# Optimization experiments

Hardware: AMD Instinct MI355X
Metric: run time of the kernel (lower is better)

Reference implementation:

```python
import jax, jax.numpy as jnp
import numpy as np

B, L, C, NH = 512, 129, 512, 8
TAU = 1.0


def layer_norm(x, g, b, eps=1e-5):
    m = x.mean(-1, keepdims=True)
    v = x.var(-1, keepdims=True)
    return (x - m) / jnp.sqrt(v + eps) * g + b


def attn_pool(tokens, query, in_w, in_b, out_w, out_b, ln_g, ln_b):
    # single-query multi-head attention pooling (nn.MultiheadAttention, batch_first)
    Bn, Ln, Cn = tokens.shape
    dh = Cn // NH
    Wq, Wk, Wv = jnp.split(in_w, 3, axis=0)
    bq, bk, bv = jnp.split(in_b, 3)
    q = (query[0, 0] @ Wq.T + bq).reshape(NH, dh)           # (H, dh), shared across batch
    k = (tokens @ Wk.T + bk).reshape(Bn, Ln, NH, dh)
    v = (tokens @ Wv.T + bv).reshape(Bn, Ln, NH, dh)
    scale = 1.0 / jnp.sqrt(jnp.asarray(dh, tokens.dtype))
    scores = jnp.einsum('hd,blhd->bhl', q, k) * scale       # (B, H, L)
    w = jax.nn.softmax(scores, axis=-1)
    out = jnp.einsum('bhl,blhd->bhd', w, v).reshape(Bn, Cn)
    out = out @ out_w.T + out_b
    return layer_norm(out, ln_g, ln_b)


def entropy(feat):
    fa = jnp.abs(feat) + 1e-8
    p = fa / fa.sum(-1, keepdims=True)
    return -(p * jnp.log(p + 1e-8)).sum(-1)


def setup_inputs() -> dict:
    key = jax.random.key(0)
    ks = jax.random.split(key, 20)
    s = C ** -0.5
    inp = {
        'rgb_tokens': jax.random.normal(ks[0], (B, L, C), jnp.float32),
        'nir_tokens': jax.random.normal(ks[1], (B, L, C), jnp.float32),
        'tir_tokens': jax.random.normal(ks[2], (B, L, C), jnp.float32),
        'rgb_query': s * jax.random.normal(ks[3], (1, 1, C), jnp.float32),
        'nir_query': s * jax.random.normal(ks[4], (1, 1, C), jnp.float32),
        'tir_query': s * jax.random.normal(ks[5], (1, 1, C), jnp.float32),
        'in_proj_w': 0.02 * jax.random.normal(ks[6], (3 * C, C), jnp.float32),
        'in_proj_b': jnp.zeros((3 * C,), jnp.float32),
        'out_proj_w': 0.02 * jax.random.normal(ks[7], (C, C), jnp.float32),
        'out_proj_b': jnp.zeros((C,), jnp.float32),
        'attn_ln_g': jnp.ones((C,), jnp.float32),
        'attn_ln_b': jnp.zeros((C,), jnp.float32),
        'ent_w': 0.02 * jax.random.normal(ks[8], (C, C), jnp.float32),
        'ent_b': jnp.zeros((C,), jnp.float32),
        'gate_w1': 0.02 * jax.random.normal(ks[9], (C, 3 * C), jnp.float32),
        'gate_b1': jnp.zeros((C,), jnp.float32),
        'gate_ln_g': jnp.ones((C,), jnp.float32),
        'gate_ln_b': jnp.zeros((C,), jnp.float32),
        'gate_w2': 0.02 * jax.random.normal(ks[10], (3, C), jnp.float32),
        'gate_b2': jnp.zeros((3,), jnp.float32),
        'alpha_raw': jnp.asarray(0.5, jnp.float32),
        'enh_w': 0.02 * jax.random.normal(ks[11], (C, C), jnp.float32),
        'enh_b': jnp.zeros((C,), jnp.float32),
        'enh_ln_g': jnp.ones((C,), jnp.float32),
        'enh_ln_b': jnp.zeros((C,), jnp.float32),
    }
    return inp


def reference(rgb_tokens, nir_tokens, tir_tokens, rgb_query, nir_query, tir_query,
              in_proj_w, in_proj_b, out_proj_w, out_proj_b, attn_ln_g, attn_ln_b,
              ent_w, ent_b, gate_w1, gate_b1, gate_ln_g, gate_ln_b, gate_w2, gate_b2,
              alpha_raw, enh_w, enh_b, enh_ln_g, enh_ln_b):
    ap = lambda t, q: attn_pool(t, q, in_proj_w, in_proj_b, out_proj_w, out_proj_b, attn_ln_g, attn_ln_b)
    h_rgb, h_nir, h_tir = ap(rgb_tokens, rgb_query), ap(nir_tokens, nir_query), ap(tir_tokens, tir_query)
    H_r, H_n, H_t = entropy(h_rgb), entropy(h_nir), entropy(h_tir)
    z = lambda h: (h @ ent_w.T + ent_b).mean(-1)
    scores = jnp.stack([z(h_rgb) * jnp.exp(-H_r / TAU),
                        z(h_nir) * jnp.exp(-H_n / TAU),
                        z(h_tir) * jnp.exp(-H_t / TAU)], axis=-1)   # (B, 3)
    ew = jax.nn.softmax(scores, axis=-1)
    h_entropy = ew[:, 0:1] * h_rgb + ew[:, 1:2] * h_nir + ew[:, 2:3] * h_tir
    h_concat = jnp.concatenate([h_rgb, h_nir, h_tir], axis=-1)      # (B, 3C)
    g = jax.nn.relu(layer_norm(h_concat @ gate_w1.T + gate_b1, gate_ln_g, gate_ln_b))
    gates = jax.nn.sigmoid(g @ gate_w2.T + gate_b2)                  # (B, 3)
    h_importance = gates[:, 0:1] * h_rgb + gates[:, 1:2] * h_nir + gates[:, 2:3] * h_tir
    alpha = jax.nn.sigmoid(alpha_raw)
    h_fused = alpha * h_entropy + (1.0 - alpha) * h_importance
    h_enh = layer_norm(h_fused @ enh_w.T + enh_b, enh_ln_g, enh_ln_b)
    return jnp.concatenate([h_rgb + h_enh, h_nir + h_enh, h_tir + h_enh], axis=-1)  # (B, 3C)
```

## Files before the change

### kernel.cpp

```cpp
#include <hip/hip_runtime.h>
#include <cstdint>

#define WS_U      0
#define WS_C0     12288
#define WS_ENTBM  12312
#define WS_ENTP   12320
#define WS_P      16416
#define WS_OUT2   WS_P
#define WS_GPRE   (WS_P + 786432)
#define WS_HFUSED (WS_P + 1572864)
#define WS_ENHPRE (WS_P + 1835008)
#define WS_VOUT   (WS_P + 6291456)
#define WS_HCAT   (WS_VOUT + 786432)
#define WS_H      (WS_HCAT + 786432)
#define WS_Z      (WS_H + 1536)

__device__ __forceinline__ float blk_sum4(float v, float* red, int lane, int wave) {
#pragma unroll
  for (int off = 32; off; off >>= 1) v += __shfl_xor(v, off);
  __syncthreads();
  if (lane == 0) red[wave] = v;
  __syncthreads();
  return red[0] + red[1] + red[2] + red[3];
}

__global__ __launch_bounds__(256) void prep_kernel(
    const float* __restrict__ qrgb, const float* __restrict__ qnir, const float* __restrict__ qtir,
    const float* __restrict__ inw, const float* __restrict__ inb,
    const float* __restrict__ entw, const float* __restrict__ entb,
    float* __restrict__ ws)
{
  const int m = blockIdx.x, h = blockIdx.y;
  const int tid = threadIdx.x, lane = tid & 63, wave = tid >> 6;
  __shared__ float qvl[64];
  __shared__ float red[4];

  if (m == 3) {
    const float* base = entw + (size_t)h * 64 * 512;
    float acc0 = 0.f, acc1 = 0.f;
#pragma unroll 8
    for (int r = 0; r < 64; r++) {
      acc0 += base[(size_t)r * 512 + tid];
      acc1 += base[(size_t)r * 512 + tid + 256];
    }
    ws[WS_ENTP + h * 512 + tid] = acc0;
    ws[WS_ENTP + h * 512 + tid + 256] = acc1;
    return;
  }

  const float* qry = (m == 0) ? qrgb : (m == 1) ? qnir : qtir;
  float4 q0 = *(const float4*)(qry + 4 * lane);
  float4 q1 = *(const float4*)(qry + 256 + 4 * lane);
#pragma unroll 4
  for (int dd = 0; dd < 16; dd++) {
    const int d = wave * 16 + dd;
    const float* wr = inw + (size_t)(h * 64 + d) * 512;
    float4 w0 = *(const float4*)(wr + 4 * lane);
    float4 w1 = *(const float4*)(wr + 256 + 4 * lane);
    float p = w0.x * q0.x + w0.y * q0.y + w0.z * q0.z + w0.w * q0.w
            + w1.x * q1.x + w1.y * q1.y + w1.z * q1.z + w1.w * q1.w;
#pragma unroll
    for (int off = 32; off; off >>= 1) p += __shfl_xor(p, off);
    if (lane == 0) qvl[d] = p + inb[h * 64 + d];
  }
  __syncthreads();
  float acc0 = 0.f, acc1 = 0.f;
  const float* wk = inw + (size_t)(512 + h * 64) * 512;
#pragma unroll 8
  for (int d = 0; d < 64; d++) {
    float qq = qvl[d];
    acc0 = fmaf(qq, wk[(size_t)d * 512 + tid], acc0);
    acc1 = fmaf(qq, wk[(size_t)d * 512 + tid + 256], acc1);
  }
  ws[WS_U + m * 4096 + h * 512 + tid] = 0.125f * acc0;
  ws[WS_U + m * 4096 + h * 512 + tid + 256] = 0.125f * acc1;
  if (m == 0 && h == 0) {
    float v = entb[tid] + entb[tid + 256];
    float s = blk_sum4(v, red, lane, wave);
    if (tid == 0) ws[WS_ENTBM] = s * (1.f / 512.f);
  }
}

__global__ __launch_bounds__(256) void attn_pool_kernel(
    const float* __restrict__ trgb, const float* __restrict__ tnir, const float* __restrict__ ttir,
    const float* __restrict__ ws, float* __restrict__ Pout)
{
  const int b = blockIdx.x, m = blockIdx.y;
  const int tid = threadIdx.x, lane = tid & 63, wave = tid >> 6;
  const float* tok = ((m == 0) ? trgb : (m == 1) ? tnir : ttir) + (size_t)b * 129 * 512;
  const float* u = ws + WS_U + m * 4096;

  __shared__ float sc[8][132];
  __shared__ float lacc[4][2][512];

  const int b0 = lane & 1, b1 = (lane >> 1) & 1, b2 = (lane >> 2) & 1;
  const int b3 = (lane >> 3) & 1, b4 = (lane >> 4) & 1;
  const int r_own = (b0 << 1) | b1;
  const int h_own = (b2 << 2) | (b3 << 1) | b4;

  const int wbase = wave * 32;

#define LOADB(L0, A0, C0, A1, C1, A2, C2, A3, C3)                         \
  do {                                                                    \
    int r0_ = (L0), r1_ = (L0) + 1, r2_ = (L0) + 2, r3_ = (L0) + 3;       \
    if (r1_ > 128) r1_ = 128;                                             \
    if (r2_ > 128) r2_ = 128;                                             \
    if (r3_ > 128) r3_ = 128;                                             \
    const float* p0_ = tok + (size_t)r0_ * 512 + 4 * lane;                \
    const float* p1_ = tok + (size_t)r1_ * 512 + 4 * lane;                \
    const float* p2_ = tok + (size_t)r2_ * 512 + 4 * lane;                \
    const float* p3_ = tok + (size_t)r3_ * 512 + 4 * lane;                \
    A0 = *(const float4*)p0_; C0 = *(const float4*)(p0_ + 256);           \
    A1 = *(const float4*)p1_; C1 = *(const float4*)(p1_ + 256);           \
    A2 = *(const float4*)p2_; C2 = *(const float4*)(p2_ + 256);           \
    A3 = *(const float4*)p3_; C3 = *(const float4*)(p3_ + 256);           \
  } while (0)

  auto score_batch = [&](int l0, bool tail,
                         float4 A0, float4 C0, float4 A1, float4 C1,
                         float4 A2, float4 C2, float4 A3, float4 C3) {
    float x[32];
#pragma unroll
    for (int h = 0; h < 8; h++) {
      float4 U0 = *(const float4*)(u + h * 512 + 4 * lane);
      float4 U1 = *(const float4*)(u + h * 512 + 256 + 4 * lane);
      x[h]      = A0.x * U0.x + A0.y * U0.y + A0.z * U0.z + A0.w * U0.w
                + C0.x * U1.x + C0.y * U1.y + C0.z * U1.z + C0.w * U1.w;
      x[8 + h]  = A1.x * U0.x + A1.y * U0.y + A1.z * U0.z + A1.w * U0.w
                + C1.x * U1.x + C1.y * U1.y + C1.z * U1.z + C1.w * U1.w;
      x[16 + h] = A2.x * U0.x + A2.y * U0.y + A2.z * U0.z + A2.w * U0.w
                + C2.x * U1.x + C2.y * U1.y + C2.z * U1.z + C2.w * U1.w;
      x[24 + h] = A3.x * U0.x + A3.y * U0.y + A3.z * U0.z + A3.w * U0.w
                + C3.x * U1.x + C3.y * U1.y + C3.z * U1.z + C3.w * U1.w;
    }
#define MERGE_STAGE(n, M, bit)                                  \
    _Pragma("unroll")                                           \
    for (int j = 0; j < (n) / 2; j++) {                         \
      float keep = (bit) ? x[j + (n) / 2] : x[j];               \
      float send = (bit) ? x[j] : x[j + (n) / 2];               \
      x[j] = keep + __shfl_xor(send, (M));                      \
    }
    MERGE_STAGE(32, 1, b0)
    MERGE_STAGE(16, 2, b1)
    MERGE_STAGE(8, 4, b2)
    MERGE_STAGE(4, 8, b3)
    MERGE_STAGE(2, 16, b4)
#undef MERGE_STAGE
    float T = x[0] + __shfl_xor(x[0], 32);
    if (lane < 32 && (!tail || r_own == 0))
      sc[h_own][l0 + r_own] = T;
  };

  {
    float4 A0, C0, A1, C1, A2, C2, A3, C3;
    float4 N0, D0, N1, D1, N2, D2, N3, D3;
    LOADB(wbase, A0, C0, A1, C1, A2, C2, A3, C3);
    for (int bt = 0; bt < 8; bt++) {
      if (bt < 7) LOADB(wbase + 4 * bt + 4, N0, D0, N1, D1, N2, D2, N3, D3);
      score_batch(wbase + 4 * bt, false, A0, C0, A1, C1, A2, C2, A3, C3);
      A0 = N0; C0 = D0; A1 = N1; C1 = D1;
      A2 = N2; C2 = D2; A3 = N3; C3 = D3;
    }
    if (wave == 0) {
      LOADB(128, A0, C0, A1, C1, A2, C2, A3, C3);
      score_batch(128, true, A0, C0, A1, C1, A2, C2, A3, C3);
    }
  }
  __syncthreads();

#pragma unroll
  for (int hh = 0; hh < 2; hh++) {
    const int h = wave * 2 + hh;
    float x0 = sc[h][lane];
    float x1 = sc[h][64 + lane];
    float x2 = (lane == 0) ? sc[h][128] : -3.0e38f;
    float mx = fmaxf(fmaxf(x0, x1), x2);
#pragma unroll
    for (int off = 32; off; off >>= 1) mx = fmaxf(mx, __shfl_xor(mx, off));
    float e0 = __expf(x0 - mx), e1 = __expf(x1 - mx);
    float e2 = (lane == 0) ? __expf(x2 - mx) : 0.f;
    float s = e0 + e1 + e2;
#pragma unroll
    for (int off = 32; off; off >>= 1) s += __shfl_xor(s, off);
    float inv = 1.f / s;
    sc[h][lane] = e0 * inv;
    sc[h][64 + lane] = e1 * inv;
    if (lane == 0) sc[h][128] = e2 * inv;
  }
  __syncthreads();

  float acc[8][8];
#pragma unroll
  for (int h = 0; h < 8; h++)
#pragma unroll
    for (int j = 0; j < 8; j++) acc[h][j] = 0.f;
  {
    float4 pa0, pc0, pa1, pc1, qa0, qc0, qa1, qc1;
    {
      const float* p0 = tok + (size_t)wbase * 512 + 4 * lane;
      const float* p1 = tok + (size_t)(wbase + 1) * 512 + 4 * lane;
      pa0 = *(const float4*)p0; pc0 = *(const float4*)(p0 + 256);
      pa1 = *(const float4*)p1; pc1 = *(const float4*)(p1 + 256);
    }
    for (int g = 0; g < 16; g++) {
      if (g < 15) {
        const float* p0 = tok + (size_t)(wbase + 2 * g + 2) * 512 + 4 * lane;
        const float* p1 = tok + (size_t)(wbase + 2 * g + 3) * 512 + 4 * lane;
        qa0 = *(const float4*)p0; qc0 = *(const float4*)(p0 + 256);
        qa1 = *(const float4*)p1; qc1 = *(const float4*)(p1 + 256);
      }
#pragma unroll
      for (int h = 0; h < 8; h++) {
        float2 w2 = *(const float2*)&sc[h][wbase + 2 * g];
        acc[h][0] = fmaf(w2.x, pa0.x, acc[h][0]);
        acc[h][1] = fmaf(w2.x, pa0.y, acc[h][1]);
        acc[h][2] = fmaf(w2.x, pa0.z, acc[h][2]);
        acc[h][3] = fmaf(w2.x, pa0.w, acc[h][3]);
        acc[h][4] = fmaf(w2.x, pc0.x, acc[h][4]);
        acc[h][5] = fmaf(w2.x, pc0.y, acc[h][5]);
        acc[h][6] = fmaf(w2.x, pc0.z, acc[h][6]);
        acc[h][7] = fmaf(w2.x, pc0.w, acc[h][7]);
        acc[h][0] = fmaf(w2.y, pa1.x, acc[h][0]);
        acc[h][1] = fmaf(w2.y, pa1.y, acc[h][1]);
        acc[h][2] = fmaf(w2.y, pa1.z, acc[h][2]);
        acc[h][3] = fmaf(w2.y, pa1.w, acc[h][3]);
        acc[h][4] = fmaf(w2.y, pc1.x, acc[h][4]);
        acc[h][5] = fmaf(w2.y, pc1.y, acc[h][5]);
        acc[h][6] = fmaf(w2.y, pc1.z, acc[h][6]);
        acc[h][7] = fmaf(w2.y, pc1.w, acc[h][7]);
      }
      pa0 = qa0; pc0 = qc0; pa1 = qa1; pc1 = qc1;
    }
    if (wave == 0) {
      const float* p0 = tok + (size_t)128 * 512 + 4 * lane;
      float4 ta = *(const float4*)p0;
      float4 tc = *(const float4*)(p0 + 256);
#pragma unroll
      for (int h = 0; h < 8; h++) {
        float wt = sc[h][128];
        acc[h][0] = fmaf(wt, ta.x, acc[h][0]);
        acc[h][1] = fmaf(wt, ta.y, acc[h][1]);
        acc[h][2] = fmaf(wt, ta.z, acc[h][2]);
        acc[h][3] = fmaf(wt, ta.w, acc[h][3]);
        acc[h][4] = fmaf(wt, tc.x, acc[h][4]);
        acc[h][5] = fmaf(wt, tc.y, acc[h][5]);
        acc[h][6] = fmaf(wt, tc.z, acc[h][6]);
        acc[h][7] = fmaf(wt, tc.w, acc[h][7]);
      }
    }
  }
#undef LOADB

  float* po = Pout + (size_t)(m * 512 + b) * 4096 + 2 * tid;
#pragma unroll
  for (int hb = 0; hb < 8; hb += 2) {
    __syncthreads();
#pragma unroll
    for (int hh = 0; hh < 2; hh++) {
      const int h = hb + hh;
      *(float4*)&lacc[wave][hh][4 * lane] =
          make_float4(acc[h][0], acc[h][1], acc[h][2], acc[h][3]);
      *(float4*)&lacc[wave][hh][256 + 4 * lane] =
          make_float4(acc[h][4], acc[h][5], acc[h][6], acc[h][7]);
    }
    __syncthreads();
#pragma unroll
    for (int hh = 0; hh < 2; hh++) {
      const int h = hb + hh;
      float2 x0 = *(const float2*)&lacc[0][hh][2 * tid];
      float2 x1 = *(const float2*)&lacc[1][hh][2 * tid];
      float2 x2 = *(const float2*)&lacc[2][hh][2 * tid];
      float2 x3 = *(const float2*)&lacc[3][hh][2 * tid];
      *(float2*)(po + h * 512) =
          make_float2(x0.x + x1.x + x2.x + x3.x, x0.y + x1.y + x2.y + x3.y);
    }
  }
}

__global__ __launch_bounds__(256) void gemm_bt_kernel(
    const float* __restrict__ A, const float* __restrict__ B,
    const float* __restrict__ bias, float* __restrict__ C,
    int K, int lda, int ldb, int ldc,
    long sA, long sB, long sC, int sBias, int addBias)
{
  A += (long)blockIdx.z * sA;
  B += (long)blockIdx.z * sB;
  C += (long)blockIdx.z * sC;
  const float* bp = bias + (long)blockIdx.z * sBias;
  __shared__ float As[32][68];
  __shared__ float Bs[32][68];
  const int tid = threadIdx.x;
  const int tx = tid & 15, ty = tid >> 4;
  const int rowL = tid >> 3;
  const int colv = (tid & 7) << 2;
  const int m0 = blockIdx.x * 64, n0 = blockIdx.y * 64;
  float acc[4][4] = {};
  for (int k0 = 0; k0 < K; k0 += 32) {
#pragma unroll
    for (int it = 0; it < 2; it++) {
      const int r = rowL + it * 32;
      float4 v = *(const float4*)(A + (size_t)(m0 + r) * lda + k0 + colv);
      As[colv + 0][r] = v.x; As[colv + 1][r] = v.y; As[colv + 2][r] = v.z; As[colv + 3][r] = v.w;
      float4 w = *(const float4*)(B + (size_t)(n0 + r) * ldb + k0 + colv);
      Bs[colv + 0][r] = w.x; Bs[colv + 1][r] = w.y; Bs[colv + 2][r] = w.z; Bs[colv + 3][r] = w.w;
    }
    __syncthreads();
#pragma unroll
    for (int k = 0; k < 32; k++) {
      float4 a4 = *(const float4*)&As[k][ty * 4];
      float4 b4 = *(const float4*)&Bs[k][tx * 4];
      acc[0][0] += a4.x * b4.x; acc[0][1] += a4.x * b4.y; acc[0][2] += a4.x * b4.z; acc[0][3] += a4.x * b4.w;
      acc[1][0] += a4.y * b4.x; acc[1][1] += a4.y * b4.y; acc[1][2] += a4.y * b4.z; acc[1][3] += a4.y * b4.w;
      acc[2][0] += a4.z * b4.x; acc[2][1] += a4.z * b4.y; acc[2][2] += a4.z * b4.z; acc[2][3] += a4.z * b4.w;
      acc[3][0] += a4.w * b4.x; acc[3][1] += a4.w * b4.y; acc[3][2] += a4.w * b4.z; acc[3][3] += a4.w * b4.w;
    }
    __syncthreads();
  }
  float4 bv = make_float4(0.f, 0.f, 0.f, 0.f);
  if (addBias) bv = *(const float4*)(bp + n0 + tx * 4);
#pragma unroll
  for (int i = 0; i < 4; i++) {
    float4 o;
    o.x = acc[i][0] + bv.x; o.y = acc[i][1] + bv.y;
    o.z = acc[i][2] + bv.z; o.w = acc[i][3] + bv.w;
    *(float4*)(C + (size_t)(m0 + ty * 4 + i) * ldc + n0 + tx * 4) = o;
  }
}

__global__ __launch_bounds__(256) void ln_ent_kernel(
    const float* __restrict__ out2,
    const float* __restrict__ lng, const float* __restrict__ lnb,
    const float* __restrict__ ws, float* __restrict__ hcat,
    float* __restrict__ Hout, float* __restrict__ zout)
{
  const int r = blockIdx.x;
  const int mod = r >> 9, b = r & 511;
  const int tid = threadIdx.x, lane = tid & 63, wave = tid >> 6;
  __shared__ float red[4];
  const float* x = out2 + (size_t)r * 512;
  float2 v = *(const float2*)(x + 2 * tid);
  float s = blk_sum4(v.x + v.y, red, lane, wave);
  float sq = blk_sum4(v.x * v.x + v.y * v.y, red, lane, wave);
  float mean = s * (1.f / 512.f);
  float var = sq * (1.f / 512.f) - mean * mean;
  float rstd = rsqrtf(var + 1e-5f);
  float2 g = *(const float2*)(lng + 2 * tid);
  float2 bb = *(const float2*)(lnb + 2 * tid);
  float h0 = (v.x - mean) * rstd * g.x + bb.x;
  float h1 = (v.y - mean) * rstd * g.y + bb.y;
  *(float2*)(hcat + (size_t)b * 1536 + mod * 512 + 2 * tid) = make_float2(h0, h1);
  float2 ep = make_float2(0.f, 0.f);
#pragma unroll
  for (int j = 0; j < 8; j++) {
    float2 t = *(const float2*)(ws + WS_ENTP + j * 512 + 2 * tid);
    ep.x += t.x; ep.y += t.y;
  }
  ep.x *= (1.f / 512.f); ep.y *= (1.f / 512.f);
  float fa0 = fabsf(h0) + 1e-8f, fa1 = fabsf(h1) + 1e-8f;
  float S = blk_sum4(fa0 + fa1, red, lane, wave);
  float zz = blk_sum4(h0 * ep.x + h1 * ep.y, red, lane, wave);
  float invS = 1.f / S;
  float p0 = fa0 * invS, p1 = fa1 * invS;
  float t = blk_sum4(p0 * logf(p0 + 1e-8f) + p1 * logf(p1 + 1e-8f), red, lane, wave);
  if (tid == 0) {
    Hout[mod * 512 + b] = -t;
    zout[mod * 512 + b] = zz + ws[WS_ENTBM];
  }
}

__global__ __launch_bounds__(256) void gate_fuse_kernel(
    const float* __restrict__ gpre, const float* __restrict__ glng, const float* __restrict__ glnb,
    const float* __restrict__ gw2, const float* __restrict__ gb2, const float* __restrict__ gb1,
    const float* __restrict__ araw, const float* __restrict__ hcat,
    const float* __restrict__ H, const float* __restrict__ z,
    float* __restrict__ hfused)
{
  const int b = blockIdx.x;
  const int tid = threadIdx.x, lane = tid & 63, wave = tid >> 6;
  __shared__ float red[4];
  float2 v;
  {
    float2 p0 = *(const float2*)(gpre + (size_t)b * 512 + 2 * tid);
    float2 p1 = *(const float2*)(gpre + 262144 + (size_t)b * 512 + 2 * tid);
    float2 p2 = *(const float2*)(gpre + 524288 + (size_t)b * 512 + 2 * tid);
    float2 bi = *(const float2*)(gb1 + 2 * tid);
    v.x = p0.x + p1.x + p2.x + bi.x;
    v.y = p0.y + p1.y + p2.y + bi.y;
  }
  float s = blk_sum4(v.x + v.y, red, lane, wave);
  float sq = blk_sum4(v.x * v.x + v.y * v.y, red, lane, wave);
  float mean = s * (1.f / 512.f), var = sq * (1.f / 512.f) - mean * mean;
  float rstd = rsqrtf(var + 1e-5f);
  float2 g = *(const float2*)(glng + 2 * tid);
  float2 bb = *(const float2*)(glnb + 2 * tid);
  float g0 = fmaxf((v.x - mean) * rstd * g.x + bb.x, 0.f);
  float g1 = fmaxf((v.y - mean) * rstd * g.y + bb.y, 0.f);
  float d0 = blk_sum4(g0 * gw2[2 * tid] + g1 * gw2[2 * tid + 1], red, lane, wave);
  float d1 = blk_sum4(g0 * gw2[512 + 2 * tid] + g1 * gw2[512 + 2 * tid + 1], red, lane, wave);
  float d2 = blk_sum4(g0 * gw2[1024 + 2 * tid] + g1 * gw2[1024 + 2 * tid + 1], red, lane, wave);
  float ga0 = 1.f / (1.f + __expf(-(d0 + gb2[0])));
  float ga1 = 1.f / (1.f + __expf(-(d1 + gb2[1])));
  float ga2 = 1.f / (1.f + __expf(-(d2 + gb2[2])));
  float sc0 = z[b] * __expf(-H[b]);
  float sc1 = z[512 + b] * __expf(-H[512 + b]);
  float sc2 = z[1024 + b] * __expf(-H[1024 + b]);
  float mxs = fmaxf(sc0, fmaxf(sc1, sc2));
  float e0 = __expf(sc0 - mxs), e1 = __expf(sc1 - mxs), e2 = __expf(sc2 - mxs);
  float inv = 1.f / (e0 + e1 + e2);
  e0 *= inv; e1 *= inv; e2 *= inv;
  float alpha = 1.f / (1.f + __expf(-araw[0]));
  const float* hb = hcat + (size_t)b * 1536 + 2 * tid;
  float2 hr = *(const float2*)hb;
  float2 hn = *(const float2*)(hb + 512);
  float2 ht = *(const float2*)(hb + 1024);
  float2 o;
  o.x = alpha * (e0 * hr.x + e1 * hn.x + e2 * ht.x)
      + (1.f - alpha) * (ga0 * hr.x + ga1 * hn.x + ga2 * ht.x);
  o.y = alpha * (e0 * hr.y + e1 * hn.y + e2 * ht.y)
      + (1.f - alpha) * (ga0 * hr.y + ga1 * hn.y + ga2 * ht.y);
  *(float2*)(hfused + (size_t)b * 512 + 2 * tid) = o;
}

__global__ __launch_bounds__(256) void final_out_kernel(
    const float* __restrict__ epre, const float* __restrict__ enb,
    const float* __restrict__ elng, const float* __restrict__ elnb,
    const float* __restrict__ hcat, float* __restrict__ out)
{
  const int b = blockIdx.x;
  const int tid = threadIdx.x, lane = tid & 63, wave = tid >> 6;
  __shared__ float red[4];
  float2 v;
  {
    float2 p0 = *(const float2*)(epre + (size_t)b * 512 + 2 * tid);
    float2 p1 = *(const float2*)(epre + 262144 + (size_t)b * 512 + 2 * tid);
    float2 bi = *(const float2*)(enb + 2 * tid);
    v.x = p0.x + p1.x + bi.x;
    v.y = p0.y + p1.y + bi.y;
  }
  float s = blk_sum4(v.x + v.y, red, lane, wave);
  float sq = blk_sum4(v.x * v.x + v.y * v.y, red, lane, wave);
  float mean = s * (1.f / 512.f), var = sq * (1.f / 512.f) - mean * mean;
  float rstd = rsqrtf(var + 1e-5f);
  float2 g = *(const float2*)(elng + 2 * tid);
  float2 bb = *(const float2*)(elnb + 2 * tid);
  float e0 = (v.x - mean) * rstd * g.x + bb.x;
  float e1 = (v.y - mean) * rstd * g.y + bb.y;
  const float* hb = hcat + (size_t)b * 1536 + 2 * tid;
  float* ob = out + (size_t)b * 1536 + 2 * tid;
#pragma unroll
  for (int mm = 0; mm < 3; mm++) {
    float2 hv = *(const float2*)(hb + mm * 512);
    *(float2*)(ob + mm * 512) = make_float2(hv.x + e0, hv.y + e1);
  }
}

extern "C" void kernel_launch(void* const* d_in, const int* in_sizes, int n_in,
                              void* d_out, int out_size, void* d_ws, size_t ws_size,
                              hipStream_t stream)
{
  const float* trgb = (const float*)d_in[0];
  const float* tnir = (const float*)d_in[1];
  const float* ttir = (const float*)d_in[2];
  const float* qrgb = (const float*)d_in[3];
  const float* qnir = (const float*)d_in[4];
  const float* qtir = (const float*)d_in[5];
  const float* inw  = (const float*)d_in[6];
  const float* inb  = (const float*)d_in[7];
  const float* outw = (const float*)d_in[8];
  const float* outb = (const float*)d_in[9];
  const float* alng = (const float*)d_in[10];
  const float* alnb = (const float*)d_in[11];
  const float* entw = (const float*)d_in[12];
  const float* entb = (const float*)d_in[13];
  const float* gw1  = (const float*)d_in[14];
  const float* gb1  = (const float*)d_in[15];
  const float* glng = (const float*)d_in[16];
  const float* glnb = (const float*)d_in[17];
  const float* gw2  = (const float*)d_in[18];
  const float* gb2  = (const float*)d_in[19];
  const float* araw = (const float*)d_in[20];
  const float* enw  = (const float*)d_in[21];
  const float* enb  = (const float*)d_in[22];
  const float* elng = (const float*)d_in[23];
  const float* elnb = (const float*)d_in[24];
  float* ws = (float*)d_ws;
  float* out = (float*)d_out;

  hipLaunchKernelGGL(prep_kernel, dim3(4, 8), dim3(256), 0, stream,
                     qrgb, qnir, qtir, inw, inb, entw, entb, ws);
  hipLaunchKernelGGL(attn_pool_kernel, dim3(512, 3), dim3(256), 0, stream,
                     trgb, tnir, ttir, ws, ws + WS_P);
  hipLaunchKernelGGL(gemm_bt_kernel, dim3(24, 1, 8), dim3(256), 0, stream,
                     ws + WS_P, inw + (size_t)1024 * 512, inb + 1024, ws + WS_VOUT,
                     512, 4096, 512, 512,
                     (long)512, (long)64 * 512, (long)64, 64, 1);
  hipLaunchKernelGGL(gemm_bt_kernel, dim3(24, 8, 1), dim3(256), 0, stream,
                     ws + WS_VOUT, outw, outb, ws + WS_OUT2,
                     512, 512, 512, 512, 0L, 0L, 0L, 0, 1);
  hipLaunchKernelGGL(ln_ent_kernel, dim3(1536), dim3(256), 0, stream,
                     ws + WS_OUT2, alng, alnb, ws, ws + WS_HCAT, ws + WS_H, ws + WS_Z);
  hipLaunchKernelGGL(gemm_bt_kernel, dim3(8, 8, 3), dim3(256), 0, stream,
                     ws + WS_HCAT, gw1, gb1, ws + WS_GPRE,
                     512, 1536, 1536, 512,
                     (long)512, (long)512, (long)262144, 0, 0);
  hipLaunchKernelGGL(gate_fuse_kernel, dim3(512), dim3(256), 0, stream,
                     ws + WS_GPRE, glng, glnb, gw2, gb2, gb1, araw,
                     ws + WS_HCAT, ws + WS_H, ws + WS_Z, ws + WS_HFUSED);
  hipLaunchKernelGGL(gemm_bt_kernel, dim3(8, 8, 2), dim3(256), 0, stream,
                     ws + WS_HFUSED, enw, enb, ws + WS_ENHPRE,
                     256, 512, 512, 512,
                     (long)256, (long)256, (long)262144, 0, 0);
  hipLaunchKernelGGL(final_out_kernel, dim3(512), dim3(256), 0, stream,
                     ws + WS_ENHPRE, enb, elng, elnb, ws + WS_HCAT, out);
}
```

Baseline: 287.5 us.

## Split attention pooling into separate score and weighted-sum kernels

The fused attention-pool kernel is split in two. The first kernel computes the scores and softmax and writes the per-head weights to the workspace. The second kernel reloads those weights and has each wave accumulate two heads over all 129 token rows. This removes the cross-wave shared-memory reduction and cuts register pressure, aiming for higher occupancy. The cost is a second full pass over the token tensors from a separate launch, plus four-fold redundant token reads per block, since every wave now streams the whole token tile.

```diff
diff --git a/kernel.cpp b/kernel.cpp
--- a/kernel.cpp
+++ b/kernel.cpp
@@ -81,7 +81,7 @@
   }
 }
 
-__global__ __launch_bounds__(256) void attn_pool_kernel(
+__global__ __launch_bounds__(256) void attn_score_kernel(
     const float* __restrict__ trgb, const float* __restrict__ tnir, const float* __restrict__ ttir,
     const float* __restrict__ ws, float* __restrict__ Pout)
 {
@@ -91,13 +91,11 @@
   const float* u = ws + WS_U + m * 4096;
 
   __shared__ float sc[8][132];
-  __shared__ float lacc[4][2][512];
 
   const int b0 = lane & 1, b1 = (lane >> 1) & 1, b2 = (lane >> 2) & 1;
   const int b3 = (lane >> 3) & 1, b4 = (lane >> 4) & 1;
   const int r_own = (b0 << 1) | b1;
   const int h_own = (b2 << 2) | (b3 << 1) | b4;
-
   const int wbase = wave * 32;
 
 #define LOADB(L0, A0, C0, A1, C1, A2, C2, A3, C3)                         \
@@ -166,8 +164,10 @@
       score_batch(128, true, A0, C0, A1, C1, A2, C2, A3, C3);
     }
   }
+#undef LOADB
   __syncthreads();
 
+  float* wout = Pout + (size_t)(m * 512 + b) * 4096;
 #pragma unroll
   for (int hh = 0; hh < 2; hh++) {
     const int h = wave * 2 + hh;
@@ -183,98 +183,80 @@
 #pragma unroll
     for (int off = 32; off; off >>= 1) s += __shfl_xor(s, off);
     float inv = 1.f / s;
-    sc[h][lane] = e0 * inv;
-    sc[h][64 + lane] = e1 * inv;
-    if (lane == 0) sc[h][128] = e2 * inv;
-  }
+    wout[h * 132 + lane] = e0 * inv;
+    wout[h * 132 + 64 + lane] = e1 * inv;
+    if (lane == 0) wout[h * 132 + 128] = e2 * inv;
+  }
+}
+
+__global__ __launch_bounds__(256) void attn_pool_kernel(
+    const float* __restrict__ trgb, const float* __restrict__ tnir, const float* __restrict__ ttir,
+    float* __restrict__ Pout)
+{
+  const int b = blockIdx.x, m = blockIdx.y;
+  const int tid = threadIdx.x, lane = tid & 63, wave = tid >> 6;
+  const float* tok = ((m == 0) ? trgb : (m == 1) ? tnir : ttir) + (size_t)b * 129 * 512;
+  float* prow = Pout + (size_t)(m * 512 + b) * 4096;
+
+  __shared__ float sc[8][132];
+  for (int i = tid; i < 1056; i += 256) ((float*)sc)[i] = prow[i];
   __syncthreads();
 
-  float acc[8][8];
-#pragma unroll
-  for (int h = 0; h < 8; h++)
-#pragma unroll
-    for (int j = 0; j < 8; j++) acc[h][j] = 0.f;
-  {
-    float4 pa0, pc0, pa1, pc1, qa0, qc0, qa1, qc1;
-    {
-      const float* p0 = tok + (size_t)wbase * 512 + 4 * lane;
-      const float* p1 = tok + (size_t)(wbase + 1) * 512 + 4 * lane;
-      pa0 = *(const float4*)p0; pc0 = *(const float4*)(p0 + 256);
-      pa1 = *(const float4*)p1; pc1 = *(const float4*)(p1 + 256);
-    }
-    for (int g = 0; g < 16; g++) {
-      if (g < 15) {
-        const float* p0 = tok + (size_t)(wbase + 2 * g + 2) * 512 + 4 * lane;
-        const float* p1 = tok + (size_t)(wbase + 2 * g + 3) * 512 + 4 * lane;
-        qa0 = *(const float4*)p0; qc0 = *(const float4*)(p0 + 256);
-        qa1 = *(const float4*)p1; qc1 = *(const float4*)(p1 + 256);
-      }
-#pragma unroll
-      for (int h = 0; h < 8; h++) {
-        float2 w2 = *(const float2*)&sc[h][wbase + 2 * g];
-        acc[h][0] = fmaf(w2.x, pa0.x, acc[h][0]);
-        acc[h][1] = fmaf(w2.x, pa0.y, acc[h][1]);
-        acc[h][2] = fmaf(w2.x, pa0.z, acc[h][2]);
-        acc[h][3] = fmaf(w2.x, pa0.w, acc[h][3]);
-        acc[h][4] = fmaf(w2.x, pc0.x, acc[h][4]);
-        acc[h][5] = fmaf(w2.x, pc0.y, acc[h][5]);
-        acc[h][6] = fmaf(w2.x, pc0.z, acc[h][6]);
-        acc[h][7] = fmaf(w2.x, pc0.w, acc[h][7]);
-        acc[h][0] = fmaf(w2.y, pa1.x, acc[h][0]);
-        acc[h][1] = fmaf(w2.y, pa1.y, acc[h][1]);
-        acc[h][2] = fmaf(w2.y, pa1.z, acc[h][2]);
-        acc[h][3] = fmaf(w2.y, pa1.w, acc[h][3]);
-        acc[h][4] = fmaf(w2.y, pc1.x, acc[h][4]);
-        acc[h][5] = fmaf(w2.y, pc1.y, acc[h][5]);
-        acc[h][6] = fmaf(w2.y, pc1.z, acc[h][6]);
-        acc[h][7] = fmaf(w2.y, pc1.w, acc[h][7]);
-      }
-      pa0 = qa0; pc0 = qc0; pa1 = qa1; pc1 = qc1;
-    }
-    if (wave == 0) {
-      const float* p0 = tok + (size_t)128 * 512 + 4 * lane;
-      float4 ta = *(const float4*)p0;
-      float4 tc = *(const float4*)(p0 + 256);
-#pragma unroll
-      for (int h = 0; h < 8; h++) {
-        float wt = sc[h][128];
-        acc[h][0] = fmaf(wt, ta.x, acc[h][0]);
-        acc[h][1] = fmaf(wt, ta.y, acc[h][1]);
-        acc[h][2] = fmaf(wt, ta.z, acc[h][2]);
-        acc[h][3] = fmaf(wt, ta.w, acc[h][3]);
-        acc[h][4] = fmaf(wt, tc.x, acc[h][4]);
-        acc[h][5] = fmaf(wt, tc.y, acc[h][5]);
-        acc[h][6] = fmaf(wt, tc.z, acc[h][6]);
-        acc[h][7] = fmaf(wt, tc.w, acc[h][7]);
-      }
-    }
-  }
-#undef LOADB
-
-  float* po = Pout + (size_t)(m * 512 + b) * 4096 + 2 * tid;
-#pragma unroll
-  for (int hb = 0; hb < 8; hb += 2) {
-    __syncthreads();
-#pragma unroll
-    for (int hh = 0; hh < 2; hh++) {
-      const int h = hb + hh;
-      *(float4*)&lacc[wave][hh][4 * lane] =
-          make_float4(acc[h][0], acc[h][1], acc[h][2], acc[h][3]);
-      *(float4*)&lacc[wave][hh][256 + 4 * lane] =
-          make_float4(acc[h][4], acc[h][5], acc[h][6], acc[h][7]);
-    }
-    __syncthreads();
-#pragma unroll
-    for (int hh = 0; hh < 2; hh++) {
-      const int h = hb + hh;
-      float2 x0 = *(const float2*)&lacc[0][hh][2 * tid];
-      float2 x1 = *(const float2*)&lacc[1][hh][2 * tid];
-      float2 x2 = *(const float2*)&lacc[2][hh][2 * tid];
-      float2 x3 = *(const float2*)&lacc[3][hh][2 * tid];
-      *(float2*)(po + h * 512) =
-          make_float2(x0.x + x1.x + x2.x + x3.x, x0.y + x1.y + x2.y + x3.y);
-    }
-  }
+  const int h0 = wave * 2, h1 = h0 + 1;
+  float4 acc00 = make_float4(0.f, 0.f, 0.f, 0.f);
+  float4 acc01 = make_float4(0.f, 0.f, 0.f, 0.f);
+  float4 acc10 = make_float4(0.f, 0.f, 0.f, 0.f);
+  float4 acc11 = make_float4(0.f, 0.f, 0.f, 0.f);
+
+#define LDROW(rr, Av, Cv)                                         \
+  do {                                                            \
+    const float* p_ = tok + (size_t)(rr) * 512 + 4 * lane;        \
+    Av = *(const float4*)p_; Cv = *(const float4*)(p_ + 256);     \
+  } while (0)
+
+#define POOLR(Av, Cv, l)                                          \
+  do {                                                            \
+    float w0_ = sc[h0][l], w1_ = sc[h1][l];                       \
+    acc00.x = fmaf(w0_, Av.x, acc00.x);                           \
+    acc00.y = fmaf(w0_, Av.y, acc00.y);                           \
+    acc00.z = fmaf(w0_, Av.z, acc00.z);                           \
+    acc00.w = fmaf(w0_, Av.w, acc00.w);                           \
+    acc01.x = fmaf(w0_, Cv.x, acc01.x);                           \
+    acc01.y = fmaf(w0_, Cv.y, acc01.y);                           \
+    acc01.z = fmaf(w0_, Cv.z, acc01.z);                           \
+    acc01.w = fmaf(w0_, Cv.w, acc01.w);                           \
+    acc10.x = fmaf(w1_, Av.x, acc10.x);                           \
+    acc10.y = fmaf(w1_, Av.y, acc10.y);                           \
+    acc10.z = fmaf(w1_, Av.z, acc10.z);                           \
+    acc10.w = fmaf(w1_, Av.w, acc10.w);                           \
+    acc11.x = fmaf(w1_, Cv.x, acc11.x);                           \
+    acc11.y = fmaf(w1_, Cv.y, acc11.y);                           \
+    acc11.z = fmaf(w1_, Cv.z, acc11.z);                           \
+    acc11.w = fmaf(w1_, Cv.w, acc11.w);                           \
+  } while (0)
+
+  float4 A0, C0, A1, C1, A2, C2, A3, C3;
+  LDROW(0, A0, C0); LDROW(1, A1, C1); LDROW(2, A2, C2); LDROW(3, A3, C3);
+  for (int g = 0; g < 32; g++) {
+    const int rb = 4 * g;
+    int rr;
+    POOLR(A0, C0, rb);
+    rr = rb + 4; if (rr > 128) rr = 128; LDROW(rr, A0, C0);
+    POOLR(A1, C1, rb + 1);
+    rr = rb + 5; if (rr > 128) rr = 128; LDROW(rr, A1, C1);
+    POOLR(A2, C2, rb + 2);
+    rr = rb + 6; if (rr > 128) rr = 128; LDROW(rr, A2, C2);
+    POOLR(A3, C3, rb + 3);
+    rr = rb + 7; if (rr > 128) rr = 128; LDROW(rr, A3, C3);
+  }
+  POOLR(A0, C0, 128);
+#undef LDROW
+#undef POOLR
+
+  *(float4*)(prow + h0 * 512 + 4 * lane) = acc00;
+  *(float4*)(prow + h0 * 512 + 256 + 4 * lane) = acc01;
+  *(float4*)(prow + h1 * 512 + 4 * lane) = acc10;
+  *(float4*)(prow + h1 * 512 + 256 + 4 * lane) = acc11;
 }
 
 __global__ __launch_bounds__(256) void gemm_bt_kernel(
@@ -488,8 +470,10 @@
 
   hipLaunchKernelGGL(prep_kernel, dim3(4, 8), dim3(256), 0, stream,
                      qrgb, qnir, qtir, inw, inb, entw, entb, ws);
+  hipLaunchKernelGGL(attn_score_kernel, dim3(512, 3), dim3(256), 0, stream,
+                     trgb, tnir, ttir, ws, ws + WS_P);
   hipLaunchKernelGGL(attn_pool_kernel, dim3(512, 3), dim3(256), 0, stream,
-                     trgb, tnir, ttir, ws, ws + WS_P);
+                     trgb, tnir, ttir, ws + WS_P);
   hipLaunchKernelGGL(gemm_bt_kernel, dim3(24, 1, 8), dim3(256), 0, stream,
                      ws + WS_P, inw + (size_t)1024 * 512, inb + 1024, ws + WS_VOUT,
                      512, 4096, 512, 512,
```

New measurement: 335.2 us. +16.6%, slower.
